# Performance work log

Hardware: AMD Instinct MI355X
Metric: run time of the kernel (lower is better)

Reference implementation:

```python
import jax, jax.numpy as jnp
import numpy as np
from jax import lax

EPS = 1e-6
BLOCK_SIZE = 64


def _feature_map(x, W):
    # x: (B,H,N,S,D), W: (H,D,F) -> (B,H,N,S,2F), computed in fp32
    u = jnp.einsum('bhnsd,hdf->bhnsf', x, W).astype(jnp.float32)
    return jnp.concatenate([jax.nn.softmax(u, axis=-1), jax.nn.softmax(-u, axis=-1)], axis=-1)


def setup_inputs() -> dict:
    key = jax.random.key(0)
    k1, k2, k3, k4, k5 = jax.random.split(key, 5)
    B, H, L, D, F = 2, 16, 4096, 64, 64
    q = jax.random.normal(k1, (B, H, L, D), dtype=jnp.float32)
    k = jax.random.normal(k2, (B, H, L, D), dtype=jnp.float32)
    v = jax.random.normal(k3, (B, H, L, D), dtype=jnp.float32)
    # hedgehog_weights initialized as eye(D,F) per head, perturbed so the test is non-trivial
    W = jnp.eye(D, F, dtype=jnp.float32)[None].repeat(H, axis=0) + 0.02 * jax.random.normal(k4, (H, D, F), dtype=jnp.float32)
    alpha = 0.1 * jax.random.normal(k5, (1, H, 1, 1), dtype=jnp.float32)
    return {"query_states": q, "key_states": k, "value_states": v,
            "hedgehog_weights": W, "alpha": alpha}


def _forward(q, k, v, W, alpha):
    B, H, L, D = q.shape
    S = BLOCK_SIZE
    N = L // S  # L chosen divisible by block size (no padding path)
    scaling = D ** (-0.5)
    F2 = 2 * W.shape[-1]

    qb = q.reshape(B, H, N, S, D)
    kb = k.reshape(B, H, N, S, D)
    vb = v.reshape(B, H, N, S, D)
    phi_q = _feature_map(qb, W)  # (B,H,N,S,2F) fp32
    phi_k = _feature_map(kb, W)
    w = jax.nn.sigmoid(alpha)    # (1,H,1,1)

    def step(carry, xs):
        S_state, Z_state = carry            # (B,H,2F,D), (B,H,2F)
        qn, kn, vn, pqn, pkn = xs           # per-block slices
        # linear-attention branch (pre-update state = clean history)
        lin_num = jnp.einsum('bhsf,bhfd->bhsd', pqn, S_state)
        lin_den = jnp.maximum(jnp.einsum('bhsf,bhf->bhs', pqn, Z_state)[..., None], EPS)
        # intra-block softmax branch (unnormalized, shared denominator)
        scores = jnp.einsum('bhsd,bhtd->bhst', qn, kn) * scaling
        a = jnp.exp(scores - scores.max(axis=-1, keepdims=True))
        sm_num = jnp.einsum('bhst,bhtd->bhsd', a, vn)
        sm_den = jnp.maximum(a.sum(axis=-1, keepdims=True), EPS)
        out = (w * sm_num + lin_num) / jnp.maximum(w * sm_den + lin_den, EPS)
        # state update with this block's keys/values
        S_state = S_state + jnp.einsum('bhsf,bhsd->bhfd', pkn, vn)
        Z_state = Z_state + pkn.sum(axis=-2)
        return (S_state, Z_state), out

    init = (jnp.zeros((B, H, F2, D), jnp.float32), jnp.zeros((B, H, F2), jnp.float32))
    xs = (jnp.moveaxis(qb, 2, 0), jnp.moveaxis(kb, 2, 0), jnp.moveaxis(vb, 2, 0),
          jnp.moveaxis(phi_q, 2, 0), jnp.moveaxis(phi_k, 2, 0))
    _, outs = lax.scan(step, init, xs)       # (N,B,H,S,D)
    return jnp.moveaxis(outs, 0, 2).reshape(B, H, L, D)


def reference(query_states, key_states, value_states, hedgehog_weights, alpha):
    return _forward(query_states, key_states, value_states, hedgehog_weights, alpha)
```

## Files before the change

kernel.cpp:

```cpp
#include <hip/hip_runtime.h>
#include <hip/hip_bf16.h>
#include <math.h>

constexpr int Hc = 16, Lc = 4096, Dc = 64;
constexpr int Nc = 64;
constexpr int F2 = 128;
constexpr int NBLK = 2048;
constexpr float EPSf = 1e-6f;
constexpr float SCALE = 0.125f;

typedef short short8 __attribute__((ext_vector_type(8)));
typedef float f32x4 __attribute__((ext_vector_type(4)));
typedef unsigned short ushort;
typedef ushort ushort4v __attribute__((ext_vector_type(4)));

__device__ inline ushort f2bf(float x) {
    return __builtin_bit_cast(ushort, __float2bfloat16(x));
}
__device__ inline float bf2f(ushort h) {
    return __builtin_bit_cast(float, ((unsigned)h) << 16);
}
__device__ inline f32x4 zero4() { f32x4 z = {0.f, 0.f, 0.f, 0.f}; return z; }

__device__ inline f32x4 mfma(short8 a, short8 b, f32x4 c) {
    return __builtin_amdgcn_mfma_f32_16x16x32_bf16(a, b, c, 0, 0, 0);
}

__device__ inline short8 ldfrag(const char* L, int row, int chunk, int rowbytes, int mask) {
    return *(const short8*)(L + row * rowbytes + ((chunk * 16) ^ ((row & mask) << 4)));
}

__device__ inline short8 gfrag_f32(const float* __restrict__ base, int row, int chunk) {
    const float4* p = (const float4*)(base + row * 64 + chunk * 8);
    float4 a = p[0], b = p[1];
    short8 r;
    r[0] = (short)f2bf(a.x); r[1] = (short)f2bf(a.y); r[2] = (short)f2bf(a.z); r[3] = (short)f2bf(a.w);
    r[4] = (short)f2bf(b.x); r[5] = (short)f2bf(b.y); r[6] = (short)f2bf(b.z); r[7] = (short)f2bf(b.w);
    return r;
}
__device__ inline short8 gfrag_bf16(const ushort* __restrict__ base, int row, int chunk, int rowlen) {
    return *(const short8*)(base + row * rowlen + chunk * 8);
}

__device__ inline void stage_rm(const float* __restrict__ src, char* dst, int t) {
    #pragma unroll
    for (int i = 0; i < 4; ++i) {
        int e = t + i * 256;
        float4 x = ((const float4*)src)[e];
        int r = e >> 4;
        int c4 = (e & 15) * 4;
        ushort4v hv;
        hv[0] = f2bf(x.x); hv[1] = f2bf(x.y); hv[2] = f2bf(x.z); hv[3] = f2bf(x.w);
        *(ushort4v*)(dst + r * 128 + ((c4 * 2) ^ ((r & 7) << 4))) = hv;
    }
}

__device__ inline void stage_tr(const float* __restrict__ src, char* dst, int t) {
    int j = t & 63, g = t >> 6;
    #pragma unroll
    for (int i = 0; i < 4; ++i) {
        int i0 = g * 4 + i * 16;
        ushort4v hv;
        #pragma unroll
        for (int jj = 0; jj < 4; ++jj) hv[jj] = f2bf(src[(i0 + jj) * 64 + j]);
        *(ushort4v*)(dst + j * 128 + ((2 * i0) ^ ((j & 7) << 4))) = hv;
    }
}

__global__ __launch_bounds__(256) void passW(const float* __restrict__ W,
                                             ushort* __restrict__ Wt)
{
    const int h = blockIdx.x, t = threadIdx.x;
    const int f = t & 63, g = t >> 6;
    const float* src = W + (long)h * 4096;
    ushort* dst = Wt + (long)h * 4096;
    #pragma unroll
    for (int i = 0; i < 16; ++i) {
        int d = g * 16 + i;
        dst[f * 64 + d] = f2bf(src[d * 64 + f]);
    }
}

__global__ __launch_bounds__(256) void passA(const float* __restrict__ K,
                                             const float* __restrict__ V,
                                             const ushort* __restrict__ Wt,
                                             ushort* __restrict__ wsS,
                                             float* __restrict__ wsZ)
{
    __shared__ __align__(16) char lds[26624];
    char* vT = lds;
    char* pT = lds + 8192;
    float* Zp = (float*)(lds + 24576);

    const int t = threadIdx.x, wv = t >> 6, l = t & 63, lr = l & 15, lg = l >> 4;
    const int bid = blockIdx.x, bh = bid >> 6, h = bh & (Hc - 1);
    const long base = (long)bh * (Lc * Dc) + (long)(bid & 63) * (64 * Dc);

    stage_tr(V + base, vT, t);

    const float* kp = K + base;
    const ushort* wt = Wt + (long)h * 4096;

    short8 ak0 = gfrag_f32(kp, 16 * wv + lr, lg);
    short8 ak1 = gfrag_f32(kp, 16 * wv + lr, 4 + lg);
    f32x4 u0[4];
    #pragma unroll
    for (int tf = 0; tf < 4; ++tf) u0[tf] = zero4();
    #pragma unroll
    for (int tf = 0; tf < 4; ++tf) {
        u0[tf] = mfma(ak0, gfrag_bf16(wt, tf * 16 + lr, lg, 64), u0[tf]);
        u0[tf] = mfma(ak1, gfrag_bf16(wt, tf * 16 + lr, 4 + lg, 64), u0[tf]);
    }

    float pp[4][4], pn[4][4];
    float zpa[4] = {0.f,0.f,0.f,0.f}, zna[4] = {0.f,0.f,0.f,0.f};
    #pragma unroll
    for (int r = 0; r < 4; ++r) {
        float sp = 0.f, sn = 0.f;
        #pragma unroll
        for (int tf = 0; tf < 4; ++tf) {
            pp[tf][r] = __expf(u0[tf][r]);  sp += pp[tf][r];
            pn[tf][r] = __expf(-u0[tf][r]); sn += pn[tf][r];
        }
        #pragma unroll
        for (int m = 1; m < 16; m <<= 1) { sp += __shfl_xor(sp, m, 16); sn += __shfl_xor(sn, m, 16); }
        float rp = 1.f / sp, rn = 1.f / sn;
        #pragma unroll
        for (int tf = 0; tf < 4; ++tf) {
            pp[tf][r] *= rp; pn[tf][r] *= rn;
            zpa[tf] += pp[tf][r]; zna[tf] += pn[tf][r];
        }
    }

    const int s0 = 16 * wv + lg * 4;
    #pragma unroll
    for (int tf = 0; tf < 4; ++tf) {
        int f = tf * 16 + lr;
        ushort4v hp, hn;
        #pragma unroll
        for (int r = 0; r < 4; ++r) { hp[r] = f2bf(pp[tf][r]); hn[r] = f2bf(pn[tf][r]); }
        *(ushort4v*)(pT + f * 128 + ((2 * s0) ^ ((f & 7) << 4))) = hp;
        int fn = 64 + f;
        *(ushort4v*)(pT + fn * 128 + ((2 * s0) ^ ((fn & 7) << 4))) = hn;
    }
    #pragma unroll
    for (int tf = 0; tf < 4; ++tf) {
        zpa[tf] += __shfl_xor(zpa[tf], 16); zpa[tf] += __shfl_xor(zpa[tf], 32);
        zna[tf] += __shfl_xor(zna[tf], 16); zna[tf] += __shfl_xor(zna[tf], 32);
    }
    if (l < 16) {
        #pragma unroll
        for (int tf = 0; tf < 4; ++tf) {
            Zp[wv * 128 + tf * 16 + lr]      = zpa[tf];
            Zp[wv * 128 + 64 + tf * 16 + lr] = zna[tf];
        }
    }
    __syncthreads();

    short8 av0 = ldfrag(vT, 16 * wv + lr, lg, 128, 7);
    short8 av1 = ldfrag(vT, 16 * wv + lr, 4 + lg, 128, 7);
    f32x4 acc[8];
    #pragma unroll
    for (int tf = 0; tf < 8; ++tf) acc[tf] = zero4();
    #pragma unroll
    for (int tf = 0; tf < 8; ++tf) {
        acc[tf] = mfma(av0, ldfrag(pT, tf * 16 + lr, lg, 128, 7), acc[tf]);
        acc[tf] = mfma(av1, ldfrag(pT, tf * 16 + lr, 4 + lg, 128, 7), acc[tf]);
    }
    ushort* o = wsS + (long)bid * (F2 * Dc);
    #pragma unroll
    for (int tf = 0; tf < 8; ++tf)
        #pragma unroll
        for (int r = 0; r < 4; ++r) {
            int d = 16 * wv + lg * 4 + r;
            o[d * 128 + tf * 16 + lr] = f2bf(acc[tf][r]);
        }

    if (t < 128)
        wsZ[(long)bid * F2 + t] = Zp[t] + Zp[128 + t] + Zp[256 + t] + Zp[384 + t];
}

__global__ __launch_bounds__(256) void passB(ushort* __restrict__ wsS,
                                             float* __restrict__ wsZ)
{
    const int t = threadIdx.x;
    if (blockIdx.x >= 256) {
        const int bh = blockIdx.x - 256;
        if (t < 128) {
            float zc = 0.f, zb[32];
            #pragma unroll
            for (int h2 = 0; h2 < 2; ++h2) {
                float* zp = wsZ + ((long)bh * 64 + h2 * 32) * 128 + t;
                #pragma unroll
                for (int i = 0; i < 32; ++i) zb[i] = zp[i * 128];
                #pragma unroll
                for (int i = 0; i < 32; ++i) { float x = zb[i]; zp[i * 128] = zc; zc += x; }
            }
        }
        return;
    }
    const int bh = blockIdx.x >> 3, chunk = blockIdx.x & 7;
    ushort* p = wsS + (long)bh * 64 * 8192 + chunk * 1024 + t * 4;
    float c0 = 0.f, c1 = 0.f, c2 = 0.f, c3 = 0.f;
    ushort4v buf[32];
    #pragma unroll
    for (int h2 = 0; h2 < 2; ++h2) {
        ushort4v* pp = (ushort4v*)(p + (long)h2 * 32 * 8192);
        #pragma unroll
        for (int i = 0; i < 32; ++i) buf[i] = pp[i * 2048];
        #pragma unroll
        for (int i = 0; i < 32; ++i) {
            ushort4v x = buf[i];
            ushort4v cc;
            cc[0] = f2bf(c0); cc[1] = f2bf(c1); cc[2] = f2bf(c2); cc[3] = f2bf(c3);
            pp[i * 2048] = cc;
            c0 += bf2f(x[0]); c1 += bf2f(x[1]); c2 += bf2f(x[2]); c3 += bf2f(x[3]);
        }
    }
}

__global__ __launch_bounds__(256) void passC(const float* __restrict__ Q,
                                             const float* __restrict__ K,
                                             const float* __restrict__ V,
                                             const ushort* __restrict__ Wt,
                                             const float* __restrict__ Alpha,
                                             const ushort* __restrict__ wsS,
                                             const float* __restrict__ wsZ,
                                             float* __restrict__ Out)
{
    __shared__ __align__(16) char lds[49664];
    char* kR    = lds;
    char* phiAB = lds;
    char* vT    = lds + 16384;
    char* St    = lds + 24576;
    char* aAB   = lds + 40960;
    float* sZ   = (float*)(lds + 49152);

    const int t = threadIdx.x, wv = t >> 6, l = t & 63, lr = l & 15, lg = l >> 4;
    const int bid = blockIdx.x, bh = bid >> 6, h = bh & (Hc - 1);
    const long base = (long)bh * (Lc * Dc) + (long)(bid & 63) * (64 * Dc);
    const int s = 16 * wv + lr;

    const float* qp = Q + base;
    short8 bq0 = gfrag_f32(qp, s, lg);
    short8 bq1 = gfrag_f32(qp, s, 4 + lg);
    const ushort* wt = Wt + (long)h * 4096;
    short8 aw[4][2];
    #pragma unroll
    for (int tf = 0; tf < 4; ++tf) {
        aw[tf][0] = gfrag_bf16(wt, tf * 16 + lr, lg, 64);
        aw[tf][1] = gfrag_bf16(wt, tf * 16 + lr, 4 + lg, 64);
    }

    {
        const short8* Sg8 = (const short8*)(wsS + (long)bid * 8192);
        #pragma unroll
        for (int i = 0; i < 4; ++i) {
            int c = t + i * 256;
            int d = c >> 4, fc = c & 15;
            *(short8*)(St + d * 256 + ((fc * 16) ^ ((d & 15) << 4))) = Sg8[c];
        }
    }
    stage_rm(K + base, kR, t);
    stage_tr(V + base, vT, t);
    if (t < 128) sZ[t] = wsZ[(long)bid * 128 + t];

    f32x4 uq[4];
    #pragma unroll
    for (int tf = 0; tf < 4; ++tf) uq[tf] = zero4();
    #pragma unroll
    for (int tf = 0; tf < 4; ++tf) {
        uq[tf] = mfma(aw[tf][0], bq0, uq[tf]);
        uq[tf] = mfma(aw[tf][1], bq1, uq[tf]);
    }
    float sp = 0.f, sn = 0.f;
    float pqp[4][4], pqn[4][4];
    #pragma unroll
    for (int tf = 0; tf < 4; ++tf)
        #pragma unroll
        for (int r = 0; r < 4; ++r) {
            pqp[tf][r] = __expf(uq[tf][r]);  sp += pqp[tf][r];
            pqn[tf][r] = __expf(-uq[tf][r]); sn += pqn[tf][r];
        }
    sp += __shfl_xor(sp, 16); sp += __shfl_xor(sp, 32);
    sn += __shfl_xor(sn, 16); sn += __shfl_xor(sn, 32);
    {
        float rp = 1.f / sp, rn = 1.f / sn;
        #pragma unroll
        for (int tf = 0; tf < 4; ++tf)
            #pragma unroll
            for (int r = 0; r < 4; ++r) { pqp[tf][r] *= rp; pqn[tf][r] *= rn; }
    }
    ushort4v phk[4], phkn[4];
    #pragma unroll
    for (int tf = 0; tf < 4; ++tf)
        #pragma unroll
        for (int r = 0; r < 4; ++r) { phk[tf][r] = f2bf(pqp[tf][r]); phkn[tf][r] = f2bf(pqn[tf][r]); }

    const float w = 1.f / (1.f + __expf(-Alpha[h]));

    __syncthreads();

    f32x4 sc[4];
    #pragma unroll
    for (int tt = 0; tt < 4; ++tt) sc[tt] = zero4();
    #pragma unroll
    for (int tt = 0; tt < 4; ++tt) {
        sc[tt] = mfma(ldfrag(kR, tt * 16 + lr, lg, 128, 7), bq0, sc[tt]);
        sc[tt] = mfma(ldfrag(kR, tt * 16 + lr, 4 + lg, 128, 7), bq1, sc[tt]);
    }
    #pragma unroll
    for (int tt = 0; tt < 4; ++tt)
        #pragma unroll
        for (int r = 0; r < 4; ++r) sc[tt][r] *= SCALE;
    float m2;
    {
        float m01 = fmaxf(fmaxf(fmaxf(sc[0][0], sc[0][1]), fmaxf(sc[0][2], sc[0][3])),
                          fmaxf(fmaxf(sc[1][0], sc[1][1]), fmaxf(sc[1][2], sc[1][3])));
        float m23 = fmaxf(fmaxf(fmaxf(sc[2][0], sc[2][1]), fmaxf(sc[2][2], sc[2][3])),
                          fmaxf(fmaxf(sc[3][0], sc[3][1]), fmaxf(sc[3][2], sc[3][3])));
        m2 = fmaxf(m01, m23);
        m2 = fmaxf(m2, __shfl_xor(m2, 16));
        m2 = fmaxf(m2, __shfl_xor(m2, 32));
    }
    float as = 0.f;
    ushort4v apk[4];
    #pragma unroll
    for (int tt = 0; tt < 4; ++tt)
        #pragma unroll
        for (int r = 0; r < 4; ++r) {
            float e = __expf(sc[tt][r] - m2);
            as += e;
            apk[tt][r] = f2bf(w * e);
        }
    as += __shfl_xor(as, 16); as += __shfl_xor(as, 32);
    const float sden = fmaxf(as, EPSf);

    float zd = 0.f;
    #pragma unroll
    for (int tf = 0; tf < 4; ++tf)
        #pragma unroll
        for (int r = 0; r < 4; ++r) {
            int f = tf * 16 + lg * 4 + r;
            zd += bf2f(phk[tf][r]) * sZ[f] + bf2f(phkn[tf][r]) * sZ[64 + f];
        }
    zd += __shfl_xor(zd, 16); zd += __shfl_xor(zd, 32);
    const float lden = fmaxf(zd, EPSf);
    const float inv = 1.f / fmaxf(w * sden + lden, EPSf);

    #pragma unroll
    for (int tt = 0; tt < 4; ++tt)
        *(ushort4v*)(aAB + s * 128 + ((32 * tt + 8 * lg) ^ ((s & 7) << 4))) = apk[tt];

    __syncthreads();

    #pragma unroll
    for (int tf = 0; tf < 4; ++tf) {
        *(ushort4v*)(phiAB + s * 256 + ((32 * tf + 8 * lg) ^ ((s & 15) << 4))) = phk[tf];
        *(ushort4v*)(phiAB + s * 256 + ((128 + 32 * tf + 8 * lg) ^ ((s & 15) << 4))) = phkn[tf];
    }

    f32x4 oacc[4];
    #pragma unroll
    for (int td = 0; td < 4; ++td) oacc[td] = zero4();
    short8 aa0 = ldfrag(aAB, s, lg, 128, 7);
    short8 aa1 = ldfrag(aAB, s, 4 + lg, 128, 7);
    #pragma unroll
    for (int td = 0; td < 4; ++td) {
        oacc[td] = mfma(aa0, ldfrag(vT, td * 16 + lr, lg, 128, 7), oacc[td]);
        oacc[td] = mfma(aa1, ldfrag(vT, td * 16 + lr, 4 + lg, 128, 7), oacc[td]);
    }
    short8 pf[4];
    #pragma unroll
    for (int kc = 0; kc < 4; ++kc) pf[kc] = ldfrag(phiAB, s, kc * 4 + lg, 256, 15);
    #pragma unroll
    for (int td = 0; td < 4; ++td)
        #pragma unroll
        for (int kc = 0; kc < 4; ++kc)
            oacc[td] = mfma(pf[kc], ldfrag(St, td * 16 + lr, kc * 4 + lg, 256, 15), oacc[td]);

    float* op = Out + base;
    #pragma unroll
    for (int r = 0; r < 4; ++r) {
        float invr = __shfl(inv, lg * 4 + r, 16);
        int sr = 16 * wv + lg * 4 + r;
        #pragma unroll
        for (int td = 0; td < 4; ++td)
            op[sr * 64 + td * 16 + lr] = oacc[td][r] * invr;
    }
}

extern "C" void kernel_launch(void* const* d_in, const int* in_sizes, int n_in,
                              void* d_out, int out_size, void* d_ws, size_t ws_size,
                              hipStream_t stream)
{
    const float* q     = (const float*)d_in[0];
    const float* k     = (const float*)d_in[1];
    const float* v     = (const float*)d_in[2];
    const float* W     = (const float*)d_in[3];
    const float* alpha = (const float*)d_in[4];
    float* out = (float*)d_out;

    ushort* wsSb = (ushort*)d_ws;
    float*  wsZ  = (float*)((char*)d_ws + (size_t)NBLK * F2 * Dc * 2);
    ushort* Wtb  = (ushort*)((char*)wsZ + (size_t)NBLK * F2 * 4);

    passW<<<Hc, 256, 0, stream>>>(W, Wtb);
    passA<<<NBLK, 256, 0, stream>>>(k, v, Wtb, wsSb, wsZ);
    passB<<<288, 256, 0, stream>>>(wsSb, wsZ);
    passC<<<NBLK, 256, 0, stream>>>(q, k, v, Wtb, alpha, wsSb, wsZ, out);
}
```

Before: 71.66 us.

## Cache bf16 transposed V from passA and DMA V/S tiles into LDS in passC

passA now writes its LDS-transposed bf16 V tile to a workspace buffer. passC loads that tile and the S state directly into LDS with global_load_lds DMA instead of re-reading fp32 V and transposing it. K fragments are loaded straight into registers rather than staged in LDS, and Z is read from global memory. This removes one barrier and sets launch bounds for three blocks per CU. The cost is an extra 16 MB workspace write/read, and correctness now depends on the S swizzle reproduced in the DMA addressing.

After: 81.14 us. +13.2%, slower.

```diff
diff --git a/kernel.cpp b/kernel.cpp
--- a/kernel.cpp
+++ b/kernel.cpp
@@ -3,7 +3,6 @@
 #include <math.h>
 
 constexpr int Hc = 16, Lc = 4096, Dc = 64;
-constexpr int Nc = 64;
 constexpr int F2 = 128;
 constexpr int NBLK = 2048;
 constexpr float EPSf = 1e-6f;
@@ -12,6 +11,7 @@
 typedef short short8 __attribute__((ext_vector_type(8)));
 typedef float f32x4 __attribute__((ext_vector_type(4)));
 typedef unsigned short ushort;
+typedef unsigned int uint;
 typedef ushort ushort4v __attribute__((ext_vector_type(4)));
 
 __device__ inline ushort f2bf(float x) {
@@ -24,6 +24,12 @@
 
 __device__ inline f32x4 mfma(short8 a, short8 b, f32x4 c) {
     return __builtin_amdgcn_mfma_f32_16x16x32_bf16(a, b, c, 0, 0, 0);
+}
+
+__device__ inline void dma16(const void* g, void* l) {
+    __builtin_amdgcn_global_load_lds(
+        (const __attribute__((address_space(1))) unsigned int*)g,
+        (__attribute__((address_space(3))) unsigned int*)l, 16, 0, 0);
 }
 
 __device__ inline short8 ldfrag(const char* L, int row, int chunk, int rowbytes, int mask) {
@@ -85,7 +91,8 @@
                                              const float* __restrict__ V,
                                              const ushort* __restrict__ Wt,
                                              ushort* __restrict__ wsS,
-                                             float* __restrict__ wsZ)
+                                             float* __restrict__ wsZ,
+                                             char* __restrict__ wsV)
 {
     __shared__ __align__(16) char lds[26624];
     char* vT = lds;
@@ -156,6 +163,13 @@
         }
     }
     __syncthreads();
+
+    {
+        const short8* vs = (const short8*)vT;
+        short8* vd = (short8*)(wsV + (long)bid * 8192);
+        vd[t]       = vs[t];
+        vd[t + 256] = vs[t + 256];
+    }
 
     short8 av0 = ldfrag(vT, 16 * wv + lr, lg, 128, 7);
     short8 av1 = ldfrag(vT, 16 * wv + lr, 4 + lg, 128, 7);
@@ -219,27 +233,42 @@
     }
 }
 
-__global__ __launch_bounds__(256) void passC(const float* __restrict__ Q,
-                                             const float* __restrict__ K,
-                                             const float* __restrict__ V,
-                                             const ushort* __restrict__ Wt,
-                                             const float* __restrict__ Alpha,
-                                             const ushort* __restrict__ wsS,
-                                             const float* __restrict__ wsZ,
-                                             float* __restrict__ Out)
+__global__ __launch_bounds__(256, 3) void passC(const float* __restrict__ Q,
+                                                const float* __restrict__ K,
+                                                const ushort* __restrict__ Wt,
+                                                const float* __restrict__ Alpha,
+                                                const ushort* __restrict__ wsS,
+                                                const float* __restrict__ wsZ,
+                                                const char* __restrict__ wsV,
+                                                float* __restrict__ Out)
 {
-    __shared__ __align__(16) char lds[49664];
-    char* kR    = lds;
-    char* phiAB = lds;
-    char* vT    = lds + 16384;
-    char* St    = lds + 24576;
+    __shared__ __align__(16) char lds[49152];
+    char* vT    = lds;
+    char* St    = lds + 8192;
+    char* phiAB = lds + 24576;
     char* aAB   = lds + 40960;
-    float* sZ   = (float*)(lds + 49152);
 
     const int t = threadIdx.x, wv = t >> 6, l = t & 63, lr = l & 15, lg = l >> 4;
     const int bid = blockIdx.x, bh = bid >> 6, h = bh & (Hc - 1);
     const long base = (long)bh * (Lc * Dc) + (long)(bid & 63) * (64 * Dc);
     const int s = 16 * wv + lr;
+
+    {
+        const char* vg = wsV + (long)bid * 8192;
+        #pragma unroll
+        for (int i = 0; i < 2; ++i) {
+            int jb = wv * 128 + i * 64;
+            dma16(vg + (long)(jb + l) * 16, vT + jb * 16);
+        }
+        const char* sg = (const char*)(wsS + (long)bid * 8192);
+        #pragma unroll
+        for (int i = 0; i < 4; ++i) {
+            int jb = wv * 256 + i * 64;
+            int j = jb + l;
+            int srcc = (j & ~15) | ((j & 15) ^ ((j >> 4) & 15));
+            dma16(sg + (long)srcc * 16, St + jb * 16);
+        }
+    }
 
     const float* qp = Q + base;
     short8 bq0 = gfrag_f32(qp, s, lg);
@@ -252,19 +281,6 @@
         aw[tf][1] = gfrag_bf16(wt, tf * 16 + lr, 4 + lg, 64);
     }
 
-    {
-        const short8* Sg8 = (const short8*)(wsS + (long)bid * 8192);
-        #pragma unroll
-        for (int i = 0; i < 4; ++i) {
-            int c = t + i * 256;
-            int d = c >> 4, fc = c & 15;
-            *(short8*)(St + d * 256 + ((fc * 16) ^ ((d & 15) << 4))) = Sg8[c];
-        }
-    }
-    stage_rm(K + base, kR, t);
-    stage_tr(V + base, vT, t);
-    if (t < 128) sZ[t] = wsZ[(long)bid * 128 + t];
-
     f32x4 uq[4];
     #pragma unroll
     for (int tf = 0; tf < 4; ++tf) uq[tf] = zero4();
@@ -273,6 +289,15 @@
         uq[tf] = mfma(aw[tf][0], bq0, uq[tf]);
         uq[tf] = mfma(aw[tf][1], bq1, uq[tf]);
     }
+
+    const float* kp = K + base;
+    short8 akf[4][2];
+    #pragma unroll
+    for (int tt = 0; tt < 4; ++tt) {
+        akf[tt][0] = gfrag_f32(kp, tt * 16 + lr, lg);
+        akf[tt][1] = gfrag_f32(kp, tt * 16 + lr, 4 + lg);
+    }
+
     float sp = 0.f, sn = 0.f;
     float pqp[4][4], pqn[4][4];
     #pragma unroll
@@ -284,30 +309,26 @@
         }
     sp += __shfl_xor(sp, 16); sp += __shfl_xor(sp, 32);
     sn += __shfl_xor(sn, 16); sn += __shfl_xor(sn, 32);
+    ushort4v phk[4], phkn[4];
     {
         float rp = 1.f / sp, rn = 1.f / sn;
         #pragma unroll
         for (int tf = 0; tf < 4; ++tf)
             #pragma unroll
-            for (int r = 0; r < 4; ++r) { pqp[tf][r] *= rp; pqn[tf][r] *= rn; }
-    }
-    ushort4v phk[4], phkn[4];
-    #pragma unroll
-    for (int tf = 0; tf < 4; ++tf)
-        #pragma unroll
-        for (int r = 0; r < 4; ++r) { phk[tf][r] = f2bf(pqp[tf][r]); phkn[tf][r] = f2bf(pqn[tf][r]); }
-
+            for (int r = 0; r < 4; ++r) {
+                phk[tf][r]  = f2bf(pqp[tf][r] * rp);
+                phkn[tf][r] = f2bf(pqn[tf][r] * rn);
+            }
+    }
     const float w = 1.f / (1.f + __expf(-Alpha[h]));
 
-    __syncthreads();
-
     f32x4 sc[4];
     #pragma unroll
     for (int tt = 0; tt < 4; ++tt) sc[tt] = zero4();
     #pragma unroll
     for (int tt = 0; tt < 4; ++tt) {
-        sc[tt] = mfma(ldfrag(kR, tt * 16 + lr, lg, 128, 7), bq0, sc[tt]);
-        sc[tt] = mfma(ldfrag(kR, tt * 16 + lr, 4 + lg, 128, 7), bq1, sc[tt]);
+        sc[tt] = mfma(akf[tt][0], bq0, sc[tt]);
+        sc[tt] = mfma(akf[tt][1], bq1, sc[tt]);
     }
     #pragma unroll
     for (int tt = 0; tt < 4; ++tt)
@@ -337,13 +358,17 @@
     const float sden = fmaxf(as, EPSf);
 
     float zd = 0.f;
-    #pragma unroll
-    for (int tf = 0; tf < 4; ++tf)
-        #pragma unroll
-        for (int r = 0; r < 4; ++r) {
-            int f = tf * 16 + lg * 4 + r;
-            zd += bf2f(phk[tf][r]) * sZ[f] + bf2f(phkn[tf][r]) * sZ[64 + f];
-        }
+    {
+        const float* zp = wsZ + (long)bid * 128;
+        #pragma unroll
+        for (int tf = 0; tf < 4; ++tf) {
+            float4 zv = *(const float4*)(zp + tf * 16 + lg * 4);
+            float4 zn = *(const float4*)(zp + 64 + tf * 16 + lg * 4);
+            #pragma unroll
+            for (int r = 0; r < 4; ++r)
+                zd += bf2f(phk[tf][r]) * (&zv.x)[r] + bf2f(phkn[tf][r]) * (&zn.x)[r];
+        }
+    }
     zd += __shfl_xor(zd, 16); zd += __shfl_xor(zd, 32);
     const float lden = fmaxf(zd, EPSf);
     const float inv = 1.f / fmaxf(w * sden + lden, EPSf);
@@ -351,14 +376,13 @@
     #pragma unroll
     for (int tt = 0; tt < 4; ++tt)
         *(ushort4v*)(aAB + s * 128 + ((32 * tt + 8 * lg) ^ ((s & 7) << 4))) = apk[tt];
-
-    __syncthreads();
-
     #pragma unroll
     for (int tf = 0; tf < 4; ++tf) {
         *(ushort4v*)(phiAB + s * 256 + ((32 * tf + 8 * lg) ^ ((s & 15) << 4))) = phk[tf];
         *(ushort4v*)(phiAB + s * 256 + ((128 + 32 * tf + 8 * lg) ^ ((s & 15) << 4))) = phkn[tf];
     }
+
+    __syncthreads();
 
     f32x4 oacc[4];
     #pragma unroll
@@ -404,9 +428,10 @@
     ushort* wsSb = (ushort*)d_ws;
     float*  wsZ  = (float*)((char*)d_ws + (size_t)NBLK * F2 * Dc * 2);
     ushort* Wtb  = (ushort*)((char*)wsZ + (size_t)NBLK * F2 * 4);
+    char*   wsV  = (char*)Wtb + (size_t)Hc * 4096 * 2;
 
     passW<<<Hc, 256, 0, stream>>>(W, Wtb);
-    passA<<<NBLK, 256, 0, stream>>>(k, v, Wtb, wsSb, wsZ);
+    passA<<<NBLK, 256, 0, stream>>>(k, v, Wtb, wsSb, wsZ, wsV);
     passB<<<288, 256, 0, stream>>>(wsSb, wsZ);
-    passC<<<NBLK, 256, 0, stream>>>(q, k, v, Wtb, alpha, wsSb, wsZ, out);
-}
+    passC<<<NBLK, 256, 0, stream>>>(q, k, Wtb, alpha, wsSb, wsZ, wsV, out);
+}
```
